# Optimization experiments

Measured on AMD Instinct MI355X. Metric: run time of the kernel, lower is better.

The kernel has to match this reference:

```python
import jax, jax.numpy as jnp
import numpy as np

NUM_ATOMS = 51
V_MIN = -10.0
V_MAX = 10.0
DELTA_Z = (V_MAX - V_MIN) / (NUM_ATOMS - 1)
Z = jnp.linspace(V_MIN, V_MAX, NUM_ATOMS)  # [num_atoms]


def setup_inputs() -> dict:
    key = jax.random.key(0)
    k1, k2, k3 = jax.random.split(key, 3)
    bs = 65536
    return {
        "logits_t": jax.random.normal(k1, (bs, NUM_ATOMS), dtype=jnp.float32),
        "logits_tp1": jax.random.normal(k2, (bs, NUM_ATOMS), dtype=jnp.float32),
        "atoms_target_t": jax.random.normal(k3, (bs, NUM_ATOMS), dtype=jnp.float32),
    }


def reference(logits_t, logits_tp1, atoms_target_t):
    probs_tp1 = jax.nn.softmax(logits_tp1, axis=-1)            # [bs, j]
    tz = jnp.clip(atoms_target_t, V_MIN, V_MAX)                # [bs, j]
    # triangular projection kernel: [bs, i, j]
    tz_z = jnp.abs(tz[:, None, :] - Z[None, :, None])
    tz_z = jnp.clip(1.0 - tz_z / DELTA_Z, 0.0, 1.0)
    probs_target_t = jnp.einsum('bij,bj->bi', tz_z, probs_tp1)
    probs_target_t = jax.lax.stop_gradient(probs_target_t)
    ce = jnp.sum(-probs_target_t * jax.nn.log_softmax(logits_t, axis=-1), axis=-1)
    return jnp.mean(ce)
```

## Files before the change

### kernel.cpp

```cpp
#include <hip/hip_runtime.h>
#include <math.h>

#define NUM_ATOMS 51
#define V_MIN_F (-10.0f)
#define V_MAX_F (10.0f)
#define INV_DELTA (2.5f)

#define GRID1 2048
#define WAVES_PER_BLOCK 4


template<int CTRL, int RM>
__device__ __forceinline__ float dpp_mov_f(float old, float x) {
    return __int_as_float(__builtin_amdgcn_update_dpp(
        __float_as_int(old), __float_as_int(x), CTRL, RM, 0xF, false));
}

__device__ __forceinline__ float wave_sum_dpp(float x) {
    x += dpp_mov_f<0x111, 0xF>(0.0f, x);
    x += dpp_mov_f<0x112, 0xF>(0.0f, x);
    x += dpp_mov_f<0x114, 0xF>(0.0f, x);
    x += dpp_mov_f<0x118, 0xF>(0.0f, x);
    x += dpp_mov_f<0x142, 0xA>(0.0f, x);
    x += dpp_mov_f<0x143, 0xC>(0.0f, x);
    return __int_as_float(__builtin_amdgcn_readlane(__float_as_int(x), 63));
}

__device__ __forceinline__ float wave_max_dpp(float x) {
    const float NI = -INFINITY;
    x = fmaxf(x, dpp_mov_f<0x111, 0xF>(NI, x));
    x = fmaxf(x, dpp_mov_f<0x112, 0xF>(NI, x));
    x = fmaxf(x, dpp_mov_f<0x114, 0xF>(NI, x));
    x = fmaxf(x, dpp_mov_f<0x118, 0xF>(NI, x));
    x = fmaxf(x, dpp_mov_f<0x142, 0xA>(NI, x));
    x = fmaxf(x, dpp_mov_f<0x143, 0xC>(NI, x));
    return __int_as_float(__builtin_amdgcn_readlane(__float_as_int(x), 63));
}

__global__ __launch_bounds__(256)
void c51_loss_stage1(const float* __restrict__ logits_t,
                     const float* __restrict__ logits_tp1,
                     const float* __restrict__ atoms_target,
                     float* __restrict__ ws,
                     int bs)
{
    const int lane  = threadIdx.x & 63;
    const int wave  = threadIdx.x >> 6;
    const int gwave = blockIdx.x * WAVES_PER_BLOCK + wave;
    const int nwave = GRID1 * WAVES_PER_BLOCK;
    const bool lane_act = (lane < NUM_ATOMS);

    float acc = 0.0f;

    for (int row = gwave; row < bs; row += nwave) {
        const long long base = (long long)row * NUM_ATOMS + lane;
        float lt   = lane_act ? logits_t[base]     : -INFINITY;
        float ltp1 = lane_act ? logits_tp1[base]   : -INFINITY;
        float at   = lane_act ? atoms_target[base] : 0.0f;

        const float m0 = wave_max_dpp(lt);
        const float m1 = wave_max_dpp(ltp1);

        const float e0 = lane_act ? __expf(lt - m0)   : 0.0f;
        const float e1 = lane_act ? __expf(ltp1 - m1) : 0.0f;

        const float s0 = wave_sum_dpp(e0);
        const float s1 = wave_sum_dpp(e1);

        const float logZ = m0 + __logf(s0);
        const float lsm  = lt - logZ;
        const float p    = e1 / s1;

        float tz = fminf(fmaxf(at, V_MIN_F), V_MAX_F);
        float x  = (tz - V_MIN_F) * INV_DELTA;
        int   i0 = (int)x;
        float frac = x - (float)i0;
        int   i1 = min(i0 + 1, NUM_ATOMS - 1);

        float g0 = __shfl(lsm, i0, 64);
        float g1 = __shfl(lsm, i1, 64);

        acc += lane_act ? p * (g0 + frac * (g1 - g0)) : 0.0f;
    }

    const float wsum = wave_sum_dpp(acc);

    __shared__ float partial[WAVES_PER_BLOCK];
    if (lane == 0) partial[wave] = wsum;
    __syncthreads();
    if (threadIdx.x == 0) {
        ws[blockIdx.x] = partial[0] + partial[1] + partial[2] + partial[3];
    }
}

__global__ __launch_bounds__(256)
void c51_loss_stage2(const float* __restrict__ ws, float* __restrict__ out,
                     int nparts, float inv_bs)
{
    const int lane = threadIdx.x & 63;
    const int wave = threadIdx.x >> 6;

    float s = 0.0f;
    for (int i = threadIdx.x; i < nparts; i += 256) s += ws[i];

    const float wsum = wave_sum_dpp(s);

    __shared__ float partial[4];
    if (lane == 0) partial[wave] = wsum;
    __syncthreads();
    if (threadIdx.x == 0) {
        float tot = partial[0] + partial[1] + partial[2] + partial[3];
        out[0] = -tot * inv_bs;
    }
}

extern "C" void kernel_launch(void* const* d_in, const int* in_sizes, int n_in,
                              void* d_out, int out_size, void* d_ws, size_t ws_size,
                              hipStream_t stream)
{
    const float* logits_t     = (const float*)d_in[0];
    const float* logits_tp1   = (const float*)d_in[1];
    const float* atoms_target = (const float*)d_in[2];
    float* out = (float*)d_out;
    float* ws  = (float*)d_ws;

    const int bs = in_sizes[0] / NUM_ATOMS;
    const float inv_bs = 1.0f / (float)bs;

    c51_loss_stage1<<<GRID1, 256, 0, stream>>>(logits_t, logits_tp1, atoms_target,
                                               ws, bs);
    c51_loss_stage2<<<1, 256, 0, stream>>>(ws, out, GRID1, inv_bs);
}
```

Measured before the change: 92.87 us.

## Drop softmax max-subtraction and restructure per-row loss into wave sums

Rewrites each row's loss algebraically as log(sum exp(lt)) minus sum(e1*interp(lt))/sum(e1). This removes both max-reductions, the per-lane log-softmax, and the cross-lane shuffles. The interpolated logits are now gathered straight from global memory, and the loop is unrolled by two. Skipping the max subtraction risks overflow in exp for large logits, and the extra gather loads may hit cache rather than registers.

```diff
diff --git a/kernel.cpp b/kernel.cpp
--- a/kernel.cpp
+++ b/kernel.cpp
@@ -9,32 +9,20 @@
 #define GRID1 2048
 #define WAVES_PER_BLOCK 4
 
-
 template<int CTRL, int RM>
 __device__ __forceinline__ float dpp_mov_f(float old, float x) {
     return __int_as_float(__builtin_amdgcn_update_dpp(
         __float_as_int(old), __float_as_int(x), CTRL, RM, 0xF, false));
 }
 
-__device__ __forceinline__ float wave_sum_dpp(float x) {
+__device__ __forceinline__ float wave_sum63(float x) {
     x += dpp_mov_f<0x111, 0xF>(0.0f, x);
     x += dpp_mov_f<0x112, 0xF>(0.0f, x);
     x += dpp_mov_f<0x114, 0xF>(0.0f, x);
     x += dpp_mov_f<0x118, 0xF>(0.0f, x);
     x += dpp_mov_f<0x142, 0xA>(0.0f, x);
     x += dpp_mov_f<0x143, 0xC>(0.0f, x);
-    return __int_as_float(__builtin_amdgcn_readlane(__float_as_int(x), 63));
-}
-
-__device__ __forceinline__ float wave_max_dpp(float x) {
-    const float NI = -INFINITY;
-    x = fmaxf(x, dpp_mov_f<0x111, 0xF>(NI, x));
-    x = fmaxf(x, dpp_mov_f<0x112, 0xF>(NI, x));
-    x = fmaxf(x, dpp_mov_f<0x114, 0xF>(NI, x));
-    x = fmaxf(x, dpp_mov_f<0x118, 0xF>(NI, x));
-    x = fmaxf(x, dpp_mov_f<0x142, 0xA>(NI, x));
-    x = fmaxf(x, dpp_mov_f<0x143, 0xC>(NI, x));
-    return __int_as_float(__builtin_amdgcn_readlane(__float_as_int(x), 63));
+    return x;
 }
 
 __global__ __launch_bounds__(256)
@@ -52,24 +40,12 @@
 
     float acc = 0.0f;
 
+    #pragma unroll 2
     for (int row = gwave; row < bs; row += nwave) {
-        const long long base = (long long)row * NUM_ATOMS + lane;
-        float lt   = lane_act ? logits_t[base]     : -INFINITY;
-        float ltp1 = lane_act ? logits_tp1[base]   : -INFINITY;
-        float at   = lane_act ? atoms_target[base] : 0.0f;
-
-        const float m0 = wave_max_dpp(lt);
-        const float m1 = wave_max_dpp(ltp1);
-
-        const float e0 = lane_act ? __expf(lt - m0)   : 0.0f;
-        const float e1 = lane_act ? __expf(ltp1 - m1) : 0.0f;
-
-        const float s0 = wave_sum_dpp(e0);
-        const float s1 = wave_sum_dpp(e1);
-
-        const float logZ = m0 + __logf(s0);
-        const float lsm  = lt - logZ;
-        const float p    = e1 / s1;
+        const size_t rbase = (size_t)row * NUM_ATOMS;
+        float lt   = lane_act ? logits_t[rbase + lane]     : 0.0f;
+        float ltp1 = lane_act ? logits_tp1[rbase + lane]   : 0.0f;
+        float at   = lane_act ? atoms_target[rbase + lane] : 0.0f;
 
         float tz = fminf(fmaxf(at, V_MIN_F), V_MAX_F);
         float x  = (tz - V_MIN_F) * INV_DELTA;
@@ -77,16 +53,23 @@
         float frac = x - (float)i0;
         int   i1 = min(i0 + 1, NUM_ATOMS - 1);
 
-        float g0 = __shfl(lsm, i0, 64);
-        float g1 = __shfl(lsm, i1, 64);
+        float g0 = logits_t[rbase + (size_t)i0];
+        float g1 = logits_t[rbase + (size_t)i1];
 
-        acc += lane_act ? p * (g0 + frac * (g1 - g0)) : 0.0f;
+        float e0 = lane_act ? __expf(lt)   : 0.0f;
+        float e1 = lane_act ? __expf(ltp1) : 0.0f;
+        float w  = e1 * (g0 + frac * (g1 - g0));
+
+        float s0 = wave_sum63(e0);
+        float s1 = wave_sum63(e1);
+        float t1 = wave_sum63(w);
+
+        float r = __logf(s0) - t1 * __builtin_amdgcn_rcpf(s1);
+        acc += (lane == 63) ? r : 0.0f;
     }
 
-    const float wsum = wave_sum_dpp(acc);
-
     __shared__ float partial[WAVES_PER_BLOCK];
-    if (lane == 0) partial[wave] = wsum;
+    if (lane == 63) partial[wave] = acc;
     __syncthreads();
     if (threadIdx.x == 0) {
         ws[blockIdx.x] = partial[0] + partial[1] + partial[2] + partial[3];
@@ -103,14 +86,14 @@
     float s = 0.0f;
     for (int i = threadIdx.x; i < nparts; i += 256) s += ws[i];
 
-    const float wsum = wave_sum_dpp(s);
+    s = wave_sum63(s);
 
     __shared__ float partial[4];
-    if (lane == 0) partial[wave] = wsum;
+    if (lane == 63) partial[wave] = s;
     __syncthreads();
     if (threadIdx.x == 0) {
         float tot = partial[0] + partial[1] + partial[2] + partial[3];
-        out[0] = -tot * inv_bs;
+        out[0] = tot * inv_bs;
     }
 }
 
```

Measured after the change: 90.35 us. -2.7%, faster.
